# Kernel tuning notes

Measured on AMD Instinct MI355X. Metric: run time of the kernel, lower is better.

The kernel has to match this reference:

```python
import jax, jax.numpy as jnp
import numpy as np

IN_F = 1024
OUT_F = 1024
GRID_SIZE = 8
GRID_LO, GRID_HI = -2.0, 2.0


def _grid_and_inv_denom():
    grid = jnp.linspace(GRID_LO, GRID_HI, GRID_SIZE)  # [G]
    inv_denom = 1.0 / (float((GRID_HI - GRID_LO) / (GRID_SIZE - 1)) + 1e-06)
    return grid, inv_denom


def setup_inputs() -> dict:
    key = jax.random.key(0)
    kx, kw, ks = jax.random.split(key, 3)
    x = jax.random.normal(kx, (4, 2048, IN_F), dtype=jnp.float32)
    # kaiming_uniform_(a=sqrt(5)) on [out,in]: bound = sqrt(6/((1+a^2)*fan_in)) = sqrt(1/fan_in)
    bound = float(np.sqrt(1.0 / IN_F))
    base_w = jax.random.uniform(kw, (OUT_F, IN_F), minval=-bound, maxval=bound, dtype=jnp.float32)
    base_b = jnp.zeros((OUT_F,), dtype=jnp.float32)
    spline_w = 0.02 * jax.random.normal(ks, (OUT_F, IN_F, GRID_SIZE), dtype=jnp.float32)
    return {"x": x, "base_w": base_w, "base_b": base_b, "spline_w": spline_w}


def reference(x, base_w, base_b, spline_w):
    grid, inv_denom = _grid_and_inv_denom()
    lead = x.shape[:-1]
    x_flat = x.reshape(-1, IN_F)  # [B, in]
    # base path: Linear(SiLU(x))
    base_out = jax.nn.silu(x_flat) @ base_w.T + base_b  # [B, out]
    # RBF basis expansion: [B, in, G]
    basis = jnp.exp(-(((x_flat[..., None] - grid) * inv_denom) ** 2))
    spline_out = jnp.einsum('big,oig->bo', basis, spline_w)  # [B, out]
    out = base_out + spline_out
    return out.reshape(*lead, OUT_F)
```

## Files before the change

kernel.cpp:

```cpp
#include <hip/hip_runtime.h>
#include <stdint.h>

namespace {

constexpr int IN_F = 1024;
constexpr int OUT_F = 1024;
constexpr int GSZ = 8;
constexpr int KTOT = IN_F + IN_F * GSZ;
constexpr int BK = 64;
constexpr int NT = KTOT / BK;
constexpr int NBASE = IN_F / BK;

constexpr int BM = 64, BN = 256;
constexpr int NBLK = OUT_F / BN;
constexpr size_t IMG_BYTES = (size_t)BN * BK * 2;
constexpr size_t WS_NEEDED = (size_t)NBLK * NT * IMG_BYTES;

constexpr double H_D     = 4.0 / 7.0;
constexpr double INVD_D  = 1.0 / (H_D + 1e-6);
constexpr double L2E_D   = 1.4426950408889634;
constexpr double SQL2E_D = 1.2011224087864498;
constexpr double CS_D    = INVD_D * SQL2E_D;
constexpr double DLT_D   = H_D * CS_D;

using short8 = __attribute__((ext_vector_type(8))) short;
using f32x4  = __attribute__((ext_vector_type(4))) float;

__device__ __forceinline__ unsigned cvt_pk(float lo, float hi) {
  unsigned r;
  asm("v_cvt_pk_bf16_f32 %0, %1, %2" : "=v"(r) : "v"(lo), "v"(hi));
  return r;
}
__device__ __forceinline__ float silu_f(float v) {
  float e = __builtin_amdgcn_exp2f(-v * (float)L2E_D);
  return v * __builtin_amdgcn_rcpf(1.0f + e);
}
__device__ __forceinline__ int swz(int row, int kk) {
  return (row * 128 + kk * 2) ^ ((row & 7) << 4);
}

__global__ void wprep(const float* __restrict__ bw, const float* __restrict__ sw,
                      char* __restrict__ wimg)
{
  const int total = NBLK * NT * BN * 8;
  for (int idx = blockIdx.x * blockDim.x + threadIdx.x; idx < total;
       idx += gridDim.x * blockDim.x) {
    const int kk8  = idx & 7;
    const int row  = (idx >> 3) & (BN - 1);
    const int rest = idx >> 11;
    const int step = rest % NT;
    const int nb   = rest / NT;
    const int o    = nb * BN + row;
    const int k    = step * BK + kk8 * 8;
    const float* src = (k < IN_F)
      ? (bw + (size_t)o * IN_F + k)
      : (sw + (size_t)o * (size_t)(IN_F * GSZ) + (k - IN_F));
    const float4 a = ((const float4*)src)[0];
    const float4 b = ((const float4*)src)[1];
    int4 v;
    v.x = (int)cvt_pk(a.x, a.y);
    v.y = (int)cvt_pk(a.z, a.w);
    v.z = (int)cvt_pk(b.x, b.y);
    v.w = (int)cvt_pk(b.z, b.w);
    *(int4*)(wimg + (size_t)rest * IMG_BYTES + swz(row, kk8 * 8)) = v;
  }
}

__global__ __launch_bounds__(256, 2)
void kan_fast(const float* __restrict__ x, const float* __restrict__ bb,
              const char* __restrict__ wimg, float* __restrict__ out)
{
  __shared__ char tA[BM * BK * 2];
  __shared__ char tB[2][BN * BK * 2];

  const int t    = threadIdx.x;
  const int lane = t & 63;
  const int wid  = t >> 6;
  const int wc   = wid * 64;
  const int bm0  = blockIdx.y * BM;
  const char* img = wimg + (size_t)blockIdx.x * NT * IMG_BYTES;
  const int bn0  = blockIdx.x * BN;

  const float CSf  = (float)CS_D;
  const float C0f  = (float)(-2.0 * CS_D);
  const float TDLT = (float)(2.0 * DLT_D);
  float Kc[7];
#pragma unroll
  for (int g = 0; g < 7; ++g) {
    const double cg  = (-2.0 + g * H_D) * CS_D;
    const double cg1 = (-2.0 + (g + 1) * H_D) * CS_D;
    Kc[g] = __builtin_amdgcn_exp2f((float)(-DLT_D * (cg + cg1)));
  }

  f32x4 acc[4][4];
#pragma unroll
  for (int m = 0; m < 4; ++m)
#pragma unroll
    for (int n = 0; n < 4; ++n) acc[m][n] = (f32x4)0.0f;

  float4 xE[4], xO[4];

  auto issue_B = [&](int step, char* dstB) {
    const char* g = img + (size_t)step * IMG_BYTES + t * 16;
    char* l = dstB + t * 16;
#pragma unroll
    for (int j = 0; j < 8; ++j)
      __builtin_amdgcn_global_load_lds(
        (const __attribute__((address_space(1))) void*)(g + j * 4096),
        (__attribute__((address_space(3))) void*)(l + j * 4096), 16, 0, 0);
  };

  auto load_x = [&](int step, float4 (&xr)[4]) {
    const int k0  = step * BK;
    const int row = t >> 2;
    if (k0 < IN_F) {
      const float* p = x + (size_t)(bm0 + row) * IN_F + k0 + (t & 3) * 16;
#pragma unroll
      for (int j = 0; j < 4; ++j) xr[j] = ((const float4*)p)[j];
    } else {
      const int i0 = (k0 - IN_F) >> 3;
      const float2 v = *(const float2*)(x + (size_t)(bm0 + row) * IN_F + i0 + (t & 3) * 2);
      xr[0].x = v.x; xr[0].y = v.y;
    }
  };

  auto conv_A = [&](int step, const float4 (&xr)[4]) {
    const int row = t >> 2;
    if (step < NBASE) {
      unsigned q[8];
#pragma unroll
      for (int j = 0; j < 4; ++j) {
        q[2 * j]     = cvt_pk(silu_f(xr[j].x), silu_f(xr[j].y));
        q[2 * j + 1] = cvt_pk(silu_f(xr[j].z), silu_f(xr[j].w));
      }
      const int kc0 = (t & 3) * 16;
      *(int4*)(tA + swz(row, kc0))     = make_int4(q[0], q[1], q[2], q[3]);
      *(int4*)(tA + swz(row, kc0 + 8)) = make_int4(q[4], q[5], q[6], q[7]);
    } else {
      float2 xv; xv.x = xr[0].x; xv.y = xr[0].y;
      float2 tb; tb.x = xv.x * CSf;        tb.y = xv.y * CSf;
      float2 d0; d0.x = tb.x - C0f;        d0.y = tb.y - C0f;
      float2 e;
      e.x = __builtin_amdgcn_exp2f(-(d0.x * d0.x));
      e.y = __builtin_amdgcn_exp2f(-(d0.y * d0.y));
      float2 r;
      r.x = __builtin_amdgcn_exp2f(tb.x * TDLT);
      r.y = __builtin_amdgcn_exp2f(tb.y * TDLT);
      unsigned q0[4], q1[4];
#pragma unroll
      for (int g = 0; g < 4; ++g) {
        float2 a = e;
        float2 b;
        b.x = a.x * r.x * Kc[2 * g];
        b.y = a.y * r.y * Kc[2 * g];
        q0[g] = cvt_pk(a.x, b.x);
        q1[g] = cvt_pk(a.y, b.y);
        if (g < 3) {
          e.x = b.x * r.x * Kc[2 * g + 1];
          e.y = b.y * r.y * Kc[2 * g + 1];
        }
      }
      const int iloc = (t & 3) * 2;
      *(int4*)(tA + swz(row, iloc * 8))       = make_int4(q0[0], q0[1], q0[2], q0[3]);
      *(int4*)(tA + swz(row, (iloc + 1) * 8)) = make_int4(q1[0], q1[1], q1[2], q1[3]);
    }
  };

  auto read_frags = [&](const char* B, int kh, short8 (&af)[4], short8 (&bf)[4]) {
    const int r  = lane & 15;
    const int kq = (lane >> 4) * 8;
#pragma unroll
    for (int m = 0; m < 4; ++m)
      af[m] = *(const short8*)(tA + swz(m * 16 + r, kh * 32 + kq));
#pragma unroll
    for (int n = 0; n < 4; ++n)
      bf[n] = *(const short8*)(B + swz(wc + n * 16 + r, kh * 32 + kq));
  };

  auto mfma16 = [&](short8 (&af)[4], short8 (&bf)[4]) {
#pragma unroll
    for (int m = 0; m < 4; ++m)
#pragma unroll
      for (int n = 0; n < 4; ++n)
        acc[m][n] = __builtin_amdgcn_mfma_f32_16x16x32_bf16(af[m], bf[n], acc[m][n], 0, 0, 0);
  };

  auto step_body = [&](int s, char* curB, char* nxtB,
                       const float4 (&xconv)[4], float4 (&xload)[4]) {
    if (s + 1 < NT) issue_B(s + 1, nxtB);
    if (s + 2 < NT) load_x(s + 2, xload);
    {
      short8 af[4], bf[4];
      read_frags(curB, 0, af, bf);
      __builtin_amdgcn_s_barrier();
      asm volatile("s_waitcnt lgkmcnt(0)" ::: "memory");
      __builtin_amdgcn_sched_barrier(0);
      __builtin_amdgcn_s_setprio(1);
      mfma16(af, bf);
      __builtin_amdgcn_s_setprio(0);
      __builtin_amdgcn_s_barrier();
    }
    {
      short8 af[4], bf[4];
      read_frags(curB, 1, af, bf);
      __builtin_amdgcn_s_barrier();
      asm volatile("s_waitcnt lgkmcnt(0)" ::: "memory");
      __builtin_amdgcn_sched_barrier(0);
      __builtin_amdgcn_s_setprio(1);
      mfma16(af, bf);
      __builtin_amdgcn_s_setprio(0);
    }
    __syncthreads();
    if (s + 1 < NT) conv_A(s + 1, xconv);
    __syncthreads();
  };

  load_x(0, xE);
  load_x(1, xO);
  issue_B(0, tB[0]);
  conv_A(0, xE);
  __syncthreads();

  for (int s = 0; s < NT; s += 2) {
    step_body(s,     tB[0], tB[1], xO, xE);
    step_body(s + 1, tB[1], tB[0], xE, xO);
  }

  const int col = lane & 15;
  const int rr  = (lane >> 4) * 4;
#pragma unroll
  for (int m = 0; m < 4; ++m) {
    const int gr = bm0 + m * 16 + rr;
#pragma unroll
    for (int n = 0; n < 4; ++n) {
      const int gc = bn0 + wc + n * 16 + col;
      const float bias = bb[gc];
#pragma unroll
      for (int j = 0; j < 4; ++j)
        out[(size_t)(gr + j) * OUT_F + gc] = acc[m][n][j] + bias;
    }
  }
}

constexpr int SLDK = 64 + 8;

__device__ __forceinline__ unsigned f2bf(float f) {
  unsigned u = __float_as_uint(f);
  return (u + 0x7fffu + ((u >> 16) & 1u)) >> 16;
}
__device__ __forceinline__ unsigned pk2(float lo, float hi) {
  return f2bf(lo) | (f2bf(hi) << 16);
}

__global__ __launch_bounds__(256)
void kan_slow(const float* __restrict__ x, const float* __restrict__ bw,
              const float* __restrict__ bb, const float* __restrict__ sw,
              float* __restrict__ out)
{
  __shared__ unsigned short tA[128][SLDK];
  __shared__ unsigned short tB[128][SLDK];

  const int t    = threadIdx.x;
  const int lane = t & 63;
  const int wid  = t >> 6;
  const int wr   = (wid >> 1) * 64;
  const int wc   = (wid & 1) * 64;
  const int bm0  = blockIdx.x * 128;
  const int bn0  = blockIdx.y * 128;

  const float CS = (float)CS_D;
  float gsc[GSZ];
#pragma unroll
  for (int g = 0; g < GSZ; ++g)
    gsc[g] = (float)((-2.0 + g * H_D) * CS_D);

  f32x4 acc[4][4];
#pragma unroll
  for (int m = 0; m < 4; ++m)
#pragma unroll
    for (int n = 0; n < 4; ++n) acc[m][n] = (f32x4)0.0f;

  float4 rA[8], rB[8];
  const int rw = t >> 4;
  const int cw = (t & 15) * 4;

  auto load_tile = [&](int step) {
    const int k0 = step * BK;
    const bool base = (k0 < IN_F);
#pragma unroll
    for (int j = 0; j < 8; ++j) {
      const int row = j * 16 + rw;
      const float* p = base
        ? (bw + (size_t)(bn0 + row) * IN_F + k0 + cw)
        : (sw + (size_t)(bn0 + row) * (size_t)(IN_F * GSZ) + (k0 - IN_F) + cw);
      rB[j] = *(const float4*)p;
    }
    if (base) {
#pragma unroll
      for (int j = 0; j < 8; ++j) {
        const int row = j * 16 + rw;
        rA[j] = *(const float4*)(x + (size_t)(bm0 + row) * IN_F + k0 + cw);
      }
    } else {
      const int i0  = (k0 - IN_F) >> 3;
      const int row = t >> 1;
      rA[0] = *(const float4*)(x + (size_t)(bm0 + row) * IN_F + i0 + (t & 1) * 4);
    }
  };

  auto store_tile = [&](int step) {
    const int k0 = step * BK;
    const bool base = (k0 < IN_F);
#pragma unroll
    for (int j = 0; j < 8; ++j) {
      const int row = j * 16 + rw;
      uint2 v;
      v.x = pk2(rB[j].x, rB[j].y);
      v.y = pk2(rB[j].z, rB[j].w);
      *(uint2*)&tB[row][cw] = v;
    }
    if (base) {
#pragma unroll
      for (int j = 0; j < 8; ++j) {
        const int row = j * 16 + rw;
        uint2 v;
        v.x = pk2(silu_f(rA[j].x), silu_f(rA[j].y));
        v.y = pk2(silu_f(rA[j].z), silu_f(rA[j].w));
        *(uint2*)&tA[row][cw] = v;
      }
    } else {
      const int row  = t >> 1;
      const int half = t & 1;
      const float* xv = (const float*)&rA[0];
#pragma unroll
      for (int c = 0; c < 4; ++c) {
        const float tb = xv[c] * CS;
        union { unsigned u[4]; int4 v4; } pkv;
#pragma unroll
        for (int g = 0; g < 8; g += 2) {
          const float t0 = tb - gsc[g];
          const float t1 = tb - gsc[g + 1];
          const float e0 = __builtin_amdgcn_exp2f(-(t0 * t0));
          const float e1 = __builtin_amdgcn_exp2f(-(t1 * t1));
          pkv.u[g >> 1] = pk2(e0, e1);
        }
        const int kc = (half * 4 + c) * 8;
        *(int4*)&tA[row][kc] = pkv.v4;
      }
    }
  };

  auto compute_tile = [&]() {
    const int r  = lane & 15;
    const int kq = (lane >> 4) * 8;
#pragma unroll
    for (int kh = 0; kh < 2; ++kh) {
      short8 af[4], bf[4];
#pragma unroll
      for (int m = 0; m < 4; ++m)
        af[m] = *(const short8*)&tA[wr + m * 16 + r][kh * 32 + kq];
#pragma unroll
      for (int n = 0; n < 4; ++n)
        bf[n] = *(const short8*)&tB[wc + n * 16 + r][kh * 32 + kq];
#pragma unroll
      for (int m = 0; m < 4; ++m)
#pragma unroll
        for (int n = 0; n < 4; ++n)
          acc[m][n] = __builtin_amdgcn_mfma_f32_16x16x32_bf16(af[m], bf[n], acc[m][n], 0, 0, 0);
    }
  };

  load_tile(0);
  for (int step = 0; step < NT; ++step) {
    store_tile(step);
    __syncthreads();
    if (step + 1 < NT) load_tile(step + 1);
    compute_tile();
    __syncthreads();
  }

  const int col = lane & 15;
  const int rr  = (lane >> 4) * 4;
#pragma unroll
  for (int m = 0; m < 4; ++m) {
    const int gr = bm0 + wr + m * 16 + rr;
#pragma unroll
    for (int n = 0; n < 4; ++n) {
      const int gc = bn0 + wc + n * 16 + col;
      const float bias = bb[gc];
#pragma unroll
      for (int j = 0; j < 4; ++j)
        out[(size_t)(gr + j) * OUT_F + gc] = acc[m][n][j] + bias;
    }
  }
}

}

extern "C" void kernel_launch(void* const* d_in, const int* in_sizes, int n_in,
                              void* d_out, int out_size, void* d_ws, size_t ws_size,
                              hipStream_t stream) {
  const float *x, *bw, *bb, *sw;
  if (in_sizes[0] == OUT_F) {
    bb = (const float*)d_in[0];
    bw = (const float*)d_in[1];
    sw = (const float*)d_in[2];
    x  = (const float*)d_in[3];
  } else {
    x  = (const float*)d_in[0];
    bw = (const float*)d_in[1];
    bb = (const float*)d_in[2];
    sw = (const float*)d_in[3];
  }
  float* out = (float*)d_out;
  const int rows = (in_sizes[0] == OUT_F) ? in_sizes[3] / IN_F : in_sizes[0] / IN_F;

  if (ws_size >= WS_NEEDED && d_ws != nullptr && (rows % BM) == 0) {
    hipLaunchKernelGGL(wprep, dim3(2048), dim3(256), 0, stream, bw, sw, (char*)d_ws);
    dim3 grid(NBLK, rows / BM);
    hipLaunchKernelGGL(kan_fast, grid, dim3(256), 0, stream,
                       x, bb, (const char*)d_ws, out);
  } else {
    dim3 grid(rows / 128, OUT_F / 128);
    hipLaunchKernelGGL(kan_slow, grid, dim3(256), 0, stream, x, bw, bb, sw, out);
  }
}
```

Before: 203.4 us.

## Double-buffer the A tile and cut per-step barriers in the GEMM main loop

The activation/basis tile in shared memory gets a second buffer, so the next step's SiLU/RBF conversion can write into the other buffer while the current step's fragments are read. Fragment reads for both k-halves are issued early and interleaved with the MFMAs. The per-step barriers drop from several to two, with an explicit vmcnt wait before the final barrier so the async B copy has landed. The cost is extra shared memory (16KB for A instead of 8KB) and tighter hand-written wait-count logic, which could be fragile.

Measured after the change: 202.9 us. About the same (-0.3%).

```diff
diff --git a/kernel.cpp b/kernel.cpp
--- a/kernel.cpp
+++ b/kernel.cpp
@@ -70,7 +70,7 @@
 void kan_fast(const float* __restrict__ x, const float* __restrict__ bb,
               const char* __restrict__ wimg, float* __restrict__ out)
 {
-  __shared__ char tA[BM * BK * 2];
+  __shared__ char tA[2][BM * BK * 2];
   __shared__ char tB[2][BN * BK * 2];
 
   const int t    = threadIdx.x;
@@ -124,7 +124,7 @@
     }
   };
 
-  auto conv_A = [&](int step, const float4 (&xr)[4]) {
+  auto conv_A = [&](int step, const float4 (&xr)[4], char* dstA) {
     const int row = t >> 2;
     if (step < NBASE) {
       unsigned q[8];
@@ -134,8 +134,8 @@
         q[2 * j + 1] = cvt_pk(silu_f(xr[j].z), silu_f(xr[j].w));
       }
       const int kc0 = (t & 3) * 16;
-      *(int4*)(tA + swz(row, kc0))     = make_int4(q[0], q[1], q[2], q[3]);
-      *(int4*)(tA + swz(row, kc0 + 8)) = make_int4(q[4], q[5], q[6], q[7]);
+      *(int4*)(dstA + swz(row, kc0))     = make_int4(q[0], q[1], q[2], q[3]);
+      *(int4*)(dstA + swz(row, kc0 + 8)) = make_int4(q[4], q[5], q[6], q[7]);
     } else {
       float2 xv; xv.x = xr[0].x; xv.y = xr[0].y;
       float2 tb; tb.x = xv.x * CSf;        tb.y = xv.y * CSf;
@@ -161,17 +161,18 @@
         }
       }
       const int iloc = (t & 3) * 2;
-      *(int4*)(tA + swz(row, iloc * 8))       = make_int4(q0[0], q0[1], q0[2], q0[3]);
-      *(int4*)(tA + swz(row, (iloc + 1) * 8)) = make_int4(q1[0], q1[1], q1[2], q1[3]);
-    }
-  };
-
-  auto read_frags = [&](const char* B, int kh, short8 (&af)[4], short8 (&bf)[4]) {
+      *(int4*)(dstA + swz(row, iloc * 8))       = make_int4(q0[0], q0[1], q0[2], q0[3]);
+      *(int4*)(dstA + swz(row, (iloc + 1) * 8)) = make_int4(q1[0], q1[1], q1[2], q1[3]);
+    }
+  };
+
+  auto read_frags = [&](const char* A, const char* B, int kh,
+                        short8 (&af)[4], short8 (&bf)[4]) {
     const int r  = lane & 15;
     const int kq = (lane >> 4) * 8;
 #pragma unroll
     for (int m = 0; m < 4; ++m)
-      af[m] = *(const short8*)(tA + swz(m * 16 + r, kh * 32 + kq));
+      af[m] = *(const short8*)(A + swz(m * 16 + r, kh * 32 + kq));
 #pragma unroll
     for (int n = 0; n < 4; ++n)
       bf[n] = *(const short8*)(B + swz(wc + n * 16 + r, kh * 32 + kq));
@@ -185,45 +186,41 @@
         acc[m][n] = __builtin_amdgcn_mfma_f32_16x16x32_bf16(af[m], bf[n], acc[m][n], 0, 0, 0);
   };
 
-  auto step_body = [&](int s, char* curB, char* nxtB,
+  auto step_body = [&](int s, char* curA, char* curB, char* nxtA, char* nxtB,
                        const float4 (&xconv)[4], float4 (&xload)[4]) {
+    short8 a0[4], b0[4], a1[4], b1[4];
+    read_frags(curA, curB, 0, a0, b0);
     if (s + 1 < NT) issue_B(s + 1, nxtB);
+    __builtin_amdgcn_sched_barrier(0);
     if (s + 2 < NT) load_x(s + 2, xload);
-    {
-      short8 af[4], bf[4];
-      read_frags(curB, 0, af, bf);
-      __builtin_amdgcn_s_barrier();
-      asm volatile("s_waitcnt lgkmcnt(0)" ::: "memory");
-      __builtin_amdgcn_sched_barrier(0);
-      __builtin_amdgcn_s_setprio(1);
-      mfma16(af, bf);
-      __builtin_amdgcn_s_setprio(0);
-      __builtin_amdgcn_s_barrier();
-    }
-    {
-      short8 af[4], bf[4];
-      read_frags(curB, 1, af, bf);
-      __builtin_amdgcn_s_barrier();
-      asm volatile("s_waitcnt lgkmcnt(0)" ::: "memory");
-      __builtin_amdgcn_sched_barrier(0);
-      __builtin_amdgcn_s_setprio(1);
-      mfma16(af, bf);
-      __builtin_amdgcn_s_setprio(0);
-    }
-    __syncthreads();
-    if (s + 1 < NT) conv_A(s + 1, xconv);
-    __syncthreads();
+    if (s + 1 < NT) conv_A(s + 1, xconv, nxtA);
+    __builtin_amdgcn_s_barrier();
+    asm volatile("s_waitcnt lgkmcnt(0)" ::: "memory");
+    __builtin_amdgcn_sched_barrier(0);
+    __builtin_amdgcn_s_setprio(1);
+    read_frags(curA, curB, 1, a1, b1);
+    mfma16(a0, b0);
+    asm volatile("s_waitcnt lgkmcnt(0)" ::: "memory");
+    __builtin_amdgcn_sched_barrier(0);
+    mfma16(a1, b1);
+    __builtin_amdgcn_s_setprio(0);
+    if (s + 2 < NT) {
+      asm volatile("s_waitcnt vmcnt(1)" ::: "memory");
+    } else {
+      asm volatile("s_waitcnt vmcnt(0)" ::: "memory");
+    }
+    __builtin_amdgcn_s_barrier();
   };
 
   load_x(0, xE);
   load_x(1, xO);
   issue_B(0, tB[0]);
-  conv_A(0, xE);
+  conv_A(0, xE, tA[0]);
   __syncthreads();
 
   for (int s = 0; s < NT; s += 2) {
-    step_body(s,     tB[0], tB[1], xO, xE);
-    step_body(s + 1, tB[1], tB[0], xE, xO);
+    step_body(s,     tA[0], tB[0], tA[1], tB[1], xO, xE);
+    step_body(s + 1, tA[1], tB[1], tA[0], tB[0], xE, xO);
   }
 
   const int col = lane & 15;
```
